# Optimization experiments

Hardware: AMD Instinct MI355X
Metric: run time of the kernel (lower is better)

Reference implementation:

```python
import jax, jax.numpy as jnp
import numpy as np
import math

N, S, D, C, CLASSES = 512, 256, 512, 1024, 1000


def setup_inputs() -> dict:
    key = jax.random.key(0)
    ks = jax.random.split(key, 9)
    q = jax.random.normal(ks[0], (N, D), dtype=jnp.float32)
    K = jax.random.normal(ks[1], (N, S, D), dtype=jnp.float32)
    V = jax.random.normal(ks[2], (N, S, D), dtype=jnp.float32)
    codebook = jax.random.normal(ks[3], (C, D), dtype=jnp.float32) / math.sqrt(D)
    Wq = jax.random.normal(ks[4], (D, D), dtype=jnp.float32) / math.sqrt(D)
    Wc = jax.random.normal(ks[5], (CLASSES, D), dtype=jnp.float32) / math.sqrt(D)
    bc = jnp.zeros((CLASSES,), dtype=jnp.float32)
    Wr = jax.random.normal(ks[6], (D, D), dtype=jnp.float32) / math.sqrt(D)
    br = jnp.zeros((D,), dtype=jnp.float32)
    return {"q": q, "K": K, "V": V, "codebook": codebook,
            "Wq": Wq, "Wc": Wc, "bc": bc, "Wr": Wr, "br": br}


def reference(q, K, V, codebook, Wq, Wc, bc, Wr, br):
    d = q.shape[-1]
    scale = math.sqrt(d)
    # query projection (Linear, no bias): q @ Wq^T
    q_proj = jnp.einsum('nd,ed->ne', q, Wq)
    # query-to-codebook soft assignment [n, c]
    code_weights = jax.nn.softmax(jnp.einsum('nd,cd->nc', q_proj, codebook) / scale, axis=-1)
    # slot-to-codebook soft assignment [n, s, c]
    slot_code_weights = jax.nn.softmax(jnp.einsum('nsd,cd->nsc', K, codebook) / scale, axis=-1)
    # fused: einsum('nc,ncd->nd', code_weights, einsum('nsc,nsd->ncd', ...))
    # == contract c first to get per-slot weights [n, s], then mix V.
    effective_weights = jnp.einsum('nc,nsc->ns', code_weights, slot_code_weights)
    summary = jnp.einsum('ns,nsd->nd', effective_weights, V)
    logits = jnp.einsum('nd,kd->nk', summary, Wc) + bc
    recon = jnp.einsum('nd,ed->ne', summary, Wr) + br
    return (logits, recon, effective_weights)
```

## Files before the change

kernel.cpp:

```cpp
#include <hip/hip_runtime.h>
#include <hip/hip_bf16.h>
#include <stdint.h>


typedef float  f32x4 __attribute__((ext_vector_type(4)));
typedef float  f32x2 __attribute__((ext_vector_type(2)));
typedef short  s16x8 __attribute__((ext_vector_type(8)));

__device__ __forceinline__ unsigned short f2bf(float x){
  unsigned u = __float_as_uint(x);
  u += 0x7fffu + ((u >> 16) & 1u);
  return (unsigned short)(u >> 16);
}
__device__ __forceinline__ float hsum4(f32x4 v){ return v[0]+v[1]+v[2]+v[3]; }

static constexpr float INV_SCALE = 0.04419417382415922f;

__global__ __launch_bounds__(256) void k_cbarr(const float* __restrict__ cb,
                                               unsigned short* __restrict__ cbB){
  const int g = blockIdx.x*256 + threadIdx.x;
  const int ks8 = g & 3;
  const int cr  = (g >> 2) & 31;
  const int kk  = (g >> 7) & 15;
  const int p   = g >> 11;
  const int c = p*32 + cr;
  const int k = kk*32 + ks8*8;
  const float* src = cb + (size_t)c*512 + k;
  const f32x4 v0 = *(const f32x4*)(src);
  const f32x4 v1 = *(const f32x4*)(src + 4);
  s16x8 o;
  o[0]=(short)f2bf(v0[0]*INV_SCALE); o[1]=(short)f2bf(v0[1]*INV_SCALE);
  o[2]=(short)f2bf(v0[2]*INV_SCALE); o[3]=(short)f2bf(v0[3]*INV_SCALE);
  o[4]=(short)f2bf(v1[0]*INV_SCALE); o[5]=(short)f2bf(v1[1]*INV_SCALE);
  o[6]=(short)f2bf(v1[2]*INV_SCALE); o[7]=(short)f2bf(v1[3]*INV_SCALE);
  *(s16x8*)(cbB + (size_t)g*8) = o;
}

__global__ __launch_bounds__(256) void k_cw(const float* __restrict__ q,
                                            const float* __restrict__ Wq,
                                            const float* __restrict__ cb,
                                            float* __restrict__ cw){
  __shared__ __align__(16) float qrow[2][512];
  __shared__ __align__(16) float qproj[2][512];
  __shared__ float ev[2][1024];
  __shared__ float red[256];
  __shared__ float tot[2];
  const int t = threadIdx.x;
  const int n0 = blockIdx.x*2;

  #pragma unroll
  for (int j = 0; j < 4; ++j){
    const int o = t + 256*j; const int ni = o >> 9, d = o & 511;
    qrow[ni][d] = q[(size_t)(n0+ni)*512 + d];
  }
  __syncthreads();

  {
    const f32x4* q0 = (const f32x4*)qrow[0];
    const f32x4* q1 = (const f32x4*)qrow[1];
    #pragma unroll 1
    for (int j = 0; j < 2; ++j){
      const int e = t + 256*j;
      const f32x4* w4 = (const f32x4*)(Wq + (size_t)e*512);
      f32x4 a0={0,0,0,0},a1={0,0,0,0};
      for (int d = 0; d < 128; ++d){
        const f32x4 wv = w4[d];
        a0 += wv*q0[d]; a1 += wv*q1[d];
      }
      qproj[0][e]=hsum4(a0); qproj[1][e]=hsum4(a1);
    }
  }
  __syncthreads();

  {
    const f32x4* p0 = (const f32x4*)qproj[0];
    const f32x4* p1 = (const f32x4*)qproj[1];
    #pragma unroll 1
    for (int j = 0; j < 4; ++j){
      const int c = t + 256*j;
      const f32x4* c4 = (const f32x4*)(cb + (size_t)c*512);
      f32x4 a0={0,0,0,0},a1={0,0,0,0};
      for (int d = 0; d < 128; ++d){
        const f32x4 wv = c4[d];
        a0 += wv*p0[d]; a1 += wv*p1[d];
      }
      ev[0][c] = __expf(hsum4(a0)*INV_SCALE);
      ev[1][c] = __expf(hsum4(a1)*INV_SCALE);
    }
  }
  __syncthreads();

  for (int ni = 0; ni < 2; ++ni){
    red[t] = ev[ni][t] + ev[ni][t+256] + ev[ni][t+512] + ev[ni][t+768];
    __syncthreads();
    for (int off = 128; off > 0; off >>= 1){
      if (t < off) red[t] += red[t+off];
      __syncthreads();
    }
    if (t == 0) tot[ni] = red[0];
    __syncthreads();
  }
  #pragma unroll
  for (int j = 0; j < 8; ++j){
    const int o = t + 256*j; const int ni = o >> 10, c = o & 1023;
    cw[(size_t)(n0+ni)*1024 + c] = ev[ni][c] / tot[ni];
  }
}

__global__ __launch_bounds__(512, 4) void k_scores(const float* __restrict__ Kt,
                                                   const unsigned short* __restrict__ cbB,
                                                   const float* __restrict__ cw,
                                                   float* __restrict__ ew_out){
  __shared__ __align__(16) short sA[64*512];
  __shared__ float cwl[1024];
  __shared__ float pe[8][64];
  __shared__ float pw[8][64];

  const int t    = threadIdx.x;
  const int lane = t & 63;
  const int w    = t >> 6;
  const int m0   = blockIdx.x * 64;
  const int n    = m0 >> 8;

  {
    const int row = t >> 3;
    const float* src = Kt + (size_t)(m0 + row) * 512;
    #pragma unroll
    for (int j = 0; j < 8; ++j){
      const int slot = (t & 7) + 8*j;
      const f32x4 v0 = *(const f32x4*)(src + slot*8);
      const f32x4 v1 = *(const f32x4*)(src + slot*8 + 4);
      s16x8 o;
      o[0]=(short)f2bf(v0[0]); o[1]=(short)f2bf(v0[1]); o[2]=(short)f2bf(v0[2]); o[3]=(short)f2bf(v0[3]);
      o[4]=(short)f2bf(v1[0]); o[5]=(short)f2bf(v1[1]); o[6]=(short)f2bf(v1[2]); o[7]=(short)f2bf(v1[3]);
      const int sp = slot ^ (row & 7);
      *(s16x8*)&sA[row*512 + sp*8] = o;
    }
  }
  cwl[t]       = cw[(size_t)n*1024 + t];
  cwl[t + 512] = cw[(size_t)n*1024 + t + 512];
  pe[w][lane] = 0.f;
  pw[w][lane] = 0.f;
  __syncthreads();

  const int kg = lane >> 4;
  const int lr = lane & 15;

  #pragma unroll 1
  for (int ci = 0; ci < 4; ++ci){
    f32x4 acc[4][2];
    #pragma unroll
    for (int fr = 0; fr < 4; ++fr)
      #pragma unroll
      for (int fc = 0; fc < 2; ++fc) acc[fr][fc] = (f32x4){0.f,0.f,0.f,0.f};

    const unsigned short* pbase = cbB + ((size_t)(ci*8 + w))*16384;
    const int loff = lr*32 + kg*8;

    s16x8 a[2][4], b[4][2];
    #pragma unroll
    for (int pk = 0; pk < 4; ++pk)
      #pragma unroll
      for (int fc = 0; fc < 2; ++fc)
        b[pk][fc] = *(const s16x8*)(pbase + (size_t)pk*1024 + fc*512 + loff);
    #pragma unroll
    for (int fr = 0; fr < 4; ++fr){
      const int row = fr*16 + lr;
      const int sp  = (0*4 + kg) ^ (row & 7);
      a[0][fr] = *(const s16x8*)&sA[row*512 + sp*8];
    }

    #pragma unroll
    for (int kk = 0; kk < 16; ++kk){
      if (kk < 13)      asm volatile("s_waitcnt vmcnt(6)" ::: "memory");
      else if (kk ==13) asm volatile("s_waitcnt vmcnt(4)" ::: "memory");
      else if (kk ==14) asm volatile("s_waitcnt vmcnt(2)" ::: "memory");
      else              asm volatile("s_waitcnt vmcnt(0)" ::: "memory");
      __builtin_amdgcn_sched_barrier(0);
      if (kk < 15){
        #pragma unroll
        for (int fr = 0; fr < 4; ++fr){
          const int row = fr*16 + lr;
          const int sp  = ((kk+1)*4 + kg) ^ (row & 7);
          a[(kk+1) & 1][fr] = *(const s16x8*)&sA[row*512 + sp*8];
        }
      }
      __builtin_amdgcn_s_setprio(1);
      #pragma unroll
      for (int fr = 0; fr < 4; ++fr)
        #pragma unroll
        for (int fc = 0; fc < 2; ++fc)
          acc[fr][fc] = __builtin_amdgcn_mfma_f32_16x16x32_bf16(a[kk & 1][fr], b[kk & 3][fc], acc[fr][fc], 0, 0, 0);
      __builtin_amdgcn_s_setprio(0);
      if (kk < 12){
        #pragma unroll
        for (int fc = 0; fc < 2; ++fc)
          b[kk & 3][fc] = *(const s16x8*)(pbase + (size_t)(kk+4)*1024 + fc*512 + loff);
      }
    }

    const float cwv0 = cwl[ci*256 + w*32 + 0*16 + lr];
    const float cwv1 = cwl[ci*256 + w*32 + 1*16 + lr];
    #pragma unroll
    for (int fr = 0; fr < 4; ++fr){
      float es[4], ws[4];
      #pragma unroll
      for (int r = 0; r < 4; ++r){
        const float e0 = __expf(acc[fr][0][r]);
        const float e1 = __expf(acc[fr][1][r]);
        es[r] = e0 + e1;
        ws[r] = e0 * cwv0 + e1 * cwv1;
      }
      #pragma unroll
      for (int r = 0; r < 4; ++r){
        float a0 = es[r], b0 = ws[r];
        #pragma unroll
        for (int m = 1; m < 16; m <<= 1){
          a0 += __shfl_xor(a0, m, 64);
          b0 += __shfl_xor(b0, m, 64);
        }
        if (lr == 0){
          const int row = fr*16 + kg*4 + r;
          pe[w][row] += a0;
          pw[w][row] += b0;
        }
      }
    }
  }

  __syncthreads();
  if (t < 64){
    float se = 0.f, sw = 0.f;
    #pragma unroll
    for (int i = 0; i < 8; ++i){ se += pe[i][t]; sw += pw[i][t]; }
    ew_out[m0 + t] = sw / se;
  }
}

__global__ __launch_bounds__(256) void k_summary(const float* __restrict__ V,
                                                 const float* __restrict__ ew,
                                                 float* __restrict__ sm){
  __shared__ float e[256];
  __shared__ f32x4 red[3][64];
  const int t = threadIdx.x;
  const int lane = t & 63, w = t >> 6;
  const int n = blockIdx.x >> 1;
  const int d0 = (blockIdx.x & 1) * 256;
  e[t] = ew[(size_t)n*256 + t];
  __syncthreads();
  const float* vb = V + (size_t)n*131072 + d0 + lane*4;
  f32x4 acc = {0.f,0.f,0.f,0.f};
  #pragma unroll 8
  for (int s = w; s < 256; s += 4){
    const f32x4 v = *(const f32x4*)(vb + (size_t)s*512);
    acc += e[s] * v;
  }
  if (w > 0) red[w-1][lane] = acc;
  __syncthreads();
  if (w == 0){
    acc += red[0][lane] + red[1][lane] + red[2][lane];
    *(f32x4*)(sm + (size_t)n*512 + d0 + lane*4) = acc;
  }
}

__global__ __launch_bounds__(256) void k_readout(const float* __restrict__ sm,
                                                 const float* __restrict__ Wc,
                                                 const float* __restrict__ bc,
                                                 const float* __restrict__ Wr,
                                                 const float* __restrict__ br,
                                                 float* __restrict__ logits,
                                                 float* __restrict__ recon){
  __shared__ __align__(16) float sl[8][512];
  const int t = threadIdx.x;
  const int nb  = blockIdx.x >> 2;
  const int wsl = blockIdx.x & 3;
  const int n0 = nb * 8;
  #pragma unroll
  for (int j = 0; j < 16; ++j){
    const int o = t + 256*j; const int ni = o >> 9, d = o & 511;
    sl[ni][d] = sm[(size_t)(n0+ni)*512 + d];
  }
  __syncthreads();
  #pragma unroll 1
  for (int j = 0; j < 2; ++j){
    const int rel = t + 256*j;
    if (rel >= 378) continue;
    const int o = wsl*378 + rel;
    const bool isl = o < 1000;
    const float* wrow = isl ? (Wc + (size_t)o*512) : (Wr + (size_t)(o-1000)*512);
    const float bias  = isl ? bc[o] : br[o-1000];
    const f32x4* w4 = (const f32x4*)wrow;
    f32x4 av[8];
    #pragma unroll
    for (int ni = 0; ni < 8; ++ni) av[ni] = (f32x4){0.f,0.f,0.f,0.f};
    for (int d = 0; d < 128; ++d){
      const f32x4 wv = w4[d];
      #pragma unroll
      for (int ni = 0; ni < 8; ++ni)
        av[ni] += wv * ((const f32x4*)sl[ni])[d];
    }
    #pragma unroll
    for (int ni = 0; ni < 8; ++ni){
      const float r = hsum4(av[ni]) + bias;
      if (isl) logits[(size_t)(n0+ni)*1000 + o] = r;
      else     recon [(size_t)(n0+ni)*512 + (o-1000)] = r;
    }
  }
}

extern "C" void kernel_launch(void* const* d_in, const int* in_sizes, int n_in,
                              void* d_out, int out_size, void* d_ws, size_t ws_size,
                              hipStream_t stream) {
  const float* q  = (const float*)d_in[0];
  const float* K  = (const float*)d_in[1];
  const float* V  = (const float*)d_in[2];
  const float* cb = (const float*)d_in[3];
  const float* Wq = (const float*)d_in[4];
  const float* Wc = (const float*)d_in[5];
  const float* bc = (const float*)d_in[6];
  const float* Wr = (const float*)d_in[7];
  const float* br = (const float*)d_in[8];

  float* out    = (float*)d_out;
  float* logits = out;
  float* recon  = out + 512*1000;
  float* ew     = out + 512*1000 + 512*512;

  char* wsb = (char*)d_ws;
  unsigned short* cbB = (unsigned short*)wsb;
  float* cw = (float*)(wsb + (1u<<20));
  float* sm = (float*)(wsb + 3u*(1u<<20));

  hipLaunchKernelGGL(k_cbarr,   dim3(256),  dim3(256), 0, stream, cb, cbB);
  hipLaunchKernelGGL(k_cw,      dim3(256),  dim3(256), 0, stream, q, Wq, cb, cw);
  hipLaunchKernelGGL(k_scores,  dim3(2048), dim3(512), 0, stream, K, cbB, cw, ew);
  hipLaunchKernelGGL(k_summary, dim3(1024), dim3(256), 0, stream, V, ew, sm);
  hipLaunchKernelGGL(k_readout, dim3(256),  dim3(256), 0, stream, sm, Wc, bc, Wr, br, logits, recon);
}
```

Baseline: 406.7 us.

## Hoist softmax partial reductions out of codebook loop and shorten B prefetch depth

Per-lane exp-sum and weighted-sum partials now accumulate in registers across all four codebook chunks, so the cross-lane shuffle reduction and the shared-memory write happen once instead of once per chunk. The B-operand global prefetch ring shrinks from four stages to two and the A-fragment LDS double buffer is removed, which lowers register pressure to make room for the accumulators. Each block also starts at a chunk offset that depends on its block index, to spread codebook reads across different addresses at any one time. The shallower prefetch and single-buffered LDS loads may expose more memory latency inside the MFMA loop.

```diff
diff --git a/kernel.cpp b/kernel.cpp
--- a/kernel.cpp
+++ b/kernel.cpp
@@ -139,15 +139,21 @@
   }
   cwl[t]       = cw[(size_t)n*1024 + t];
   cwl[t + 512] = cw[(size_t)n*1024 + t + 512];
-  pe[w][lane] = 0.f;
-  pw[w][lane] = 0.f;
   __syncthreads();
 
   const int kg = lane >> 4;
   const int lr = lane & 15;
+  const int rot = blockIdx.x & 3;
+
+  float es[4][4], ws[4][4];
+  #pragma unroll
+  for (int fr = 0; fr < 4; ++fr)
+    #pragma unroll
+    for (int r = 0; r < 4; ++r){ es[fr][r] = 0.f; ws[fr][r] = 0.f; }
 
   #pragma unroll 1
-  for (int ci = 0; ci < 4; ++ci){
+  for (int p = 0; p < 4; ++p){
+    const int ci = (p + rot) & 3;
     f32x4 acc[4][2];
     #pragma unroll
     for (int fr = 0; fr < 4; ++fr)
@@ -157,45 +163,37 @@
     const unsigned short* pbase = cbB + ((size_t)(ci*8 + w))*16384;
     const int loff = lr*32 + kg*8;
 
-    s16x8 a[2][4], b[4][2];
-    #pragma unroll
-    for (int pk = 0; pk < 4; ++pk)
-      #pragma unroll
-      for (int fc = 0; fc < 2; ++fc)
-        b[pk][fc] = *(const s16x8*)(pbase + (size_t)pk*1024 + fc*512 + loff);
-    #pragma unroll
-    for (int fr = 0; fr < 4; ++fr){
-      const int row = fr*16 + lr;
-      const int sp  = (0*4 + kg) ^ (row & 7);
-      a[0][fr] = *(const s16x8*)&sA[row*512 + sp*8];
-    }
+    s16x8 a[4], b[2][2];
+    #pragma unroll
+    for (int fc = 0; fc < 2; ++fc)
+      b[0][fc] = *(const s16x8*)(pbase + 0*1024 + fc*512 + loff);
+    #pragma unroll
+    for (int fc = 0; fc < 2; ++fc)
+      b[1][fc] = *(const s16x8*)(pbase + 1*1024 + fc*512 + loff);
 
     #pragma unroll
     for (int kk = 0; kk < 16; ++kk){
-      if (kk < 13)      asm volatile("s_waitcnt vmcnt(6)" ::: "memory");
-      else if (kk ==13) asm volatile("s_waitcnt vmcnt(4)" ::: "memory");
-      else if (kk ==14) asm volatile("s_waitcnt vmcnt(2)" ::: "memory");
-      else              asm volatile("s_waitcnt vmcnt(0)" ::: "memory");
+      if (kk < 15) asm volatile("s_waitcnt vmcnt(2)" ::: "memory");
+      else         asm volatile("s_waitcnt vmcnt(0)" ::: "memory");
       __builtin_amdgcn_sched_barrier(0);
-      if (kk < 15){
-        #pragma unroll
-        for (int fr = 0; fr < 4; ++fr){
-          const int row = fr*16 + lr;
-          const int sp  = ((kk+1)*4 + kg) ^ (row & 7);
-          a[(kk+1) & 1][fr] = *(const s16x8*)&sA[row*512 + sp*8];
-        }
+      #pragma unroll
+      for (int fr = 0; fr < 4; ++fr){
+        const int row = fr*16 + lr;
+        const int sp  = (kk*4 + kg) ^ (row & 7);
+        a[fr] = *(const s16x8*)&sA[row*512 + sp*8];
       }
       __builtin_amdgcn_s_setprio(1);
       #pragma unroll
       for (int fr = 0; fr < 4; ++fr)
         #pragma unroll
         for (int fc = 0; fc < 2; ++fc)
-          acc[fr][fc] = __builtin_amdgcn_mfma_f32_16x16x32_bf16(a[kk & 1][fr], b[kk & 3][fc], acc[fr][fc], 0, 0, 0);
+          acc[fr][fc] = __builtin_amdgcn_mfma_f32_16x16x32_bf16(a[fr], b[kk & 1][fc], acc[fr][fc], 0, 0, 0);
       __builtin_amdgcn_s_setprio(0);
-      if (kk < 12){
+      __builtin_amdgcn_sched_barrier(0);
+      if (kk < 14){
         #pragma unroll
         for (int fc = 0; fc < 2; ++fc)
-          b[kk & 3][fc] = *(const s16x8*)(pbase + (size_t)(kk+4)*1024 + fc*512 + loff);
+          b[kk & 1][fc] = *(const s16x8*)(pbase + (size_t)(kk+2)*1024 + fc*512 + loff);
       }
     }
 
@@ -203,27 +201,30 @@
     const float cwv1 = cwl[ci*256 + w*32 + 1*16 + lr];
     #pragma unroll
     for (int fr = 0; fr < 4; ++fr){
-      float es[4], ws[4];
       #pragma unroll
       for (int r = 0; r < 4; ++r){
         const float e0 = __expf(acc[fr][0][r]);
         const float e1 = __expf(acc[fr][1][r]);
-        es[r] = e0 + e1;
-        ws[r] = e0 * cwv0 + e1 * cwv1;
-      }
-      #pragma unroll
-      for (int r = 0; r < 4; ++r){
-        float a0 = es[r], b0 = ws[r];
-        #pragma unroll
-        for (int m = 1; m < 16; m <<= 1){
-          a0 += __shfl_xor(a0, m, 64);
-          b0 += __shfl_xor(b0, m, 64);
-        }
-        if (lr == 0){
-          const int row = fr*16 + kg*4 + r;
-          pe[w][row] += a0;
-          pw[w][row] += b0;
-        }
+        es[fr][r] += e0 + e1;
+        ws[fr][r] += e0 * cwv0 + e1 * cwv1;
+      }
+    }
+  }
+
+  #pragma unroll
+  for (int fr = 0; fr < 4; ++fr){
+    #pragma unroll
+    for (int r = 0; r < 4; ++r){
+      float a0 = es[fr][r], b0 = ws[fr][r];
+      #pragma unroll
+      for (int m = 1; m < 16; m <<= 1){
+        a0 += __shfl_xor(a0, m, 64);
+        b0 += __shfl_xor(b0, m, 64);
+      }
+      if (lr == 0){
+        const int row = fr*16 + kg*4 + r;
+        pe[w][row] = a0;
+        pw[w][row] = b0;
       }
     }
   }
```

New measurement: 387.1 us. -4.8%, faster.

## Widen codebook tile per wave to 64 columns and re-pipeline B loads

Applied to the files above, without the earlier changes.

The codebook pre-layout now packs 64 codes per panel instead of 32. The slot-codebook GEMM loop processes two 64-wide chunks instead of four 32-wide ones, so each A fragment read from LDS feeds twice as many MFMAs. The B-fragment prefetch becomes a split double-buffer (b0/b1) with tighter vmcnt waits, and the start chunk is rotated by block parity to spread L2 traffic. This halves LDS A reads and the number of epilogue shuffle reductions, at the cost of more accumulator registers and a shallower global-load prefetch depth.

```diff
diff --git a/kernel.cpp b/kernel.cpp
--- a/kernel.cpp
+++ b/kernel.cpp
@@ -20,10 +20,10 @@
                                                unsigned short* __restrict__ cbB){
   const int g = blockIdx.x*256 + threadIdx.x;
   const int ks8 = g & 3;
-  const int cr  = (g >> 2) & 31;
-  const int kk  = (g >> 7) & 15;
-  const int p   = g >> 11;
-  const int c = p*32 + cr;
+  const int cr  = (g >> 2) & 63;
+  const int kk  = (g >> 8) & 15;
+  const int p   = g >> 12;
+  const int c = p*64 + cr;
   const int k = kk*32 + ks8*8;
   const float* src = cb + (size_t)c*512 + k;
   const f32x4 v0 = *(const f32x4*)(src);
@@ -145,84 +145,93 @@
 
   const int kg = lane >> 4;
   const int lr = lane & 15;
+  const int rot = blockIdx.x & 1;
 
   #pragma unroll 1
-  for (int ci = 0; ci < 4; ++ci){
-    f32x4 acc[4][2];
+  for (int p = 0; p < 2; ++p){
+    const int ci = p ^ rot;
+    f32x4 acc[4][4];
     #pragma unroll
     for (int fr = 0; fr < 4; ++fr)
       #pragma unroll
-      for (int fc = 0; fc < 2; ++fc) acc[fr][fc] = (f32x4){0.f,0.f,0.f,0.f};
-
-    const unsigned short* pbase = cbB + ((size_t)(ci*8 + w))*16384;
+      for (int fc = 0; fc < 4; ++fc) acc[fr][fc] = (f32x4){0.f,0.f,0.f,0.f};
+
+    const unsigned short* pbase = cbB + ((size_t)(ci*8 + w))*32768;
     const int loff = lr*32 + kg*8;
 
-    s16x8 a[2][4], b[4][2];
-    #pragma unroll
-    for (int pk = 0; pk < 4; ++pk)
-      #pragma unroll
-      for (int fc = 0; fc < 2; ++fc)
-        b[pk][fc] = *(const s16x8*)(pbase + (size_t)pk*1024 + fc*512 + loff);
-    #pragma unroll
-    for (int fr = 0; fr < 4; ++fr){
-      const int row = fr*16 + lr;
-      const int sp  = (0*4 + kg) ^ (row & 7);
-      a[0][fr] = *(const s16x8*)&sA[row*512 + sp*8];
-    }
+    s16x8 a[4], b0[2], b1[2];
+    b0[0] = *(const s16x8*)(pbase + 0*2048 + 0*512 + loff);
+    b0[1] = *(const s16x8*)(pbase + 0*2048 + 1*512 + loff);
+    b1[0] = *(const s16x8*)(pbase + 0*2048 + 2*512 + loff);
+    b1[1] = *(const s16x8*)(pbase + 0*2048 + 3*512 + loff);
 
     #pragma unroll
     for (int kk = 0; kk < 16; ++kk){
-      if (kk < 13)      asm volatile("s_waitcnt vmcnt(6)" ::: "memory");
-      else if (kk ==13) asm volatile("s_waitcnt vmcnt(4)" ::: "memory");
-      else if (kk ==14) asm volatile("s_waitcnt vmcnt(2)" ::: "memory");
-      else              asm volatile("s_waitcnt vmcnt(0)" ::: "memory");
+      #pragma unroll
+      for (int fr = 0; fr < 4; ++fr){
+        const int row = fr*16 + lr;
+        const int sp  = (kk*4 + kg) ^ (row & 7);
+        a[fr] = *(const s16x8*)&sA[row*512 + sp*8];
+      }
+      asm volatile("s_waitcnt vmcnt(2)" ::: "memory");
+      __builtin_amdgcn_sched_barrier(0);
+      __builtin_amdgcn_s_setprio(1);
+      #pragma unroll
+      for (int fr = 0; fr < 4; ++fr)
+        #pragma unroll
+        for (int h = 0; h < 2; ++h)
+          acc[fr][h] = __builtin_amdgcn_mfma_f32_16x16x32_bf16(a[fr], b0[h], acc[fr][h], 0, 0, 0);
+      __builtin_amdgcn_s_setprio(0);
       __builtin_amdgcn_sched_barrier(0);
       if (kk < 15){
-        #pragma unroll
-        for (int fr = 0; fr < 4; ++fr){
-          const int row = fr*16 + lr;
-          const int sp  = ((kk+1)*4 + kg) ^ (row & 7);
-          a[(kk+1) & 1][fr] = *(const s16x8*)&sA[row*512 + sp*8];
-        }
-      }
+        b0[0] = *(const s16x8*)(pbase + (size_t)(kk+1)*2048 + 0*512 + loff);
+        b0[1] = *(const s16x8*)(pbase + (size_t)(kk+1)*2048 + 1*512 + loff);
+        asm volatile("s_waitcnt vmcnt(2)" ::: "memory");
+      } else {
+        asm volatile("s_waitcnt vmcnt(0)" ::: "memory");
+      }
+      __builtin_amdgcn_sched_barrier(0);
       __builtin_amdgcn_s_setprio(1);
       #pragma unroll
       for (int fr = 0; fr < 4; ++fr)
         #pragma unroll
-        for (int fc = 0; fc < 2; ++fc)
-          acc[fr][fc] = __builtin_amdgcn_mfma_f32_16x16x32_bf16(a[kk & 1][fr], b[kk & 3][fc], acc[fr][fc], 0, 0, 0);
+        for (int h = 0; h < 2; ++h)
+          acc[fr][2+h] = __builtin_amdgcn_mfma_f32_16x16x32_bf16(a[fr], b1[h], acc[fr][2+h], 0, 0, 0);
       __builtin_amdgcn_s_setprio(0);
-      if (kk < 12){
+      __builtin_amdgcn_sched_barrier(0);
+      if (kk < 15){
+        b1[0] = *(const s16x8*)(pbase + (size_t)(kk+1)*2048 + 2*512 + loff);
+        b1[1] = *(const s16x8*)(pbase + (size_t)(kk+1)*2048 + 3*512 + loff);
+      }
+    }
+
+    float cwv[4];
+    #pragma unroll
+    for (int fc = 0; fc < 4; ++fc) cwv[fc] = cwl[ci*512 + w*64 + fc*16 + lr];
+    #pragma unroll
+    for (int fr = 0; fr < 4; ++fr){
+      float es[4] = {0,0,0,0}, ws[4] = {0,0,0,0};
+      #pragma unroll
+      for (int fc = 0; fc < 4; ++fc){
         #pragma unroll
-        for (int fc = 0; fc < 2; ++fc)
-          b[kk & 3][fc] = *(const s16x8*)(pbase + (size_t)(kk+4)*1024 + fc*512 + loff);
-      }
-    }
-
-    const float cwv0 = cwl[ci*256 + w*32 + 0*16 + lr];
-    const float cwv1 = cwl[ci*256 + w*32 + 1*16 + lr];
-    #pragma unroll
-    for (int fr = 0; fr < 4; ++fr){
-      float es[4], ws[4];
+        for (int r = 0; r < 4; ++r){
+          const float e = __expf(acc[fr][fc][r]);
+          es[r] += e;
+          ws[r] += e * cwv[fc];
+        }
+      }
       #pragma unroll
       for (int r = 0; r < 4; ++r){
-        const float e0 = __expf(acc[fr][0][r]);
-        const float e1 = __expf(acc[fr][1][r]);
-        es[r] = e0 + e1;
-        ws[r] = e0 * cwv0 + e1 * cwv1;
-      }
-      #pragma unroll
-      for (int r = 0; r < 4; ++r){
-        float a0 = es[r], b0 = ws[r];
+        float a0 = es[r], b0r = ws[r];
         #pragma unroll
         for (int m = 1; m < 16; m <<= 1){
-          a0 += __shfl_xor(a0, m, 64);
-          b0 += __shfl_xor(b0, m, 64);
+          a0  += __shfl_xor(a0, m, 64);
+          b0r += __shfl_xor(b0r, m, 64);
         }
         if (lr == 0){
           const int row = fr*16 + kg*4 + r;
           pe[w][row] += a0;
-          pw[w][row] += b0;
+          pw[w][row] += b0r;
         }
       }
     }
```

After: 407.5 us. Within noise of the previous version (+0.2%).
